# Optimization experiments

Measured on AMD Instinct MI355X. Metric: run time of the kernel, lower is better.

The kernel has to match this reference:

```python
import jax, jax.numpy as jnp
import numpy as np

B, N, F, H, L = 8, 4096, 240, 32, 240


def setup_inputs() -> dict:
    key = jax.random.key(0)
    k_x, k_a, k_w1, k_w2 = jax.random.split(key, 4)
    x = jax.random.normal(k_x, (B, N, F), dtype=jnp.float32)
    a = jax.random.uniform(k_a, (N, N), dtype=jnp.float32)
    W1 = jax.random.normal(k_w1, (F, H), dtype=jnp.float32) * (1.0 / np.sqrt(F))
    b1 = jnp.zeros((H,), dtype=jnp.float32)
    W2 = jax.random.normal(k_w2, (H, L), dtype=jnp.float32) * (1.0 / np.sqrt(H))
    b2 = jnp.zeros((L,), dtype=jnp.float32)
    return {"x": x, "a": a, "W1": W1, "b1": b1, "W2": W2, "b2": b2}


def reference(x, a, W1, b1, W2, b2):
    # GCNConv: transform features first (cheap), then aggregate over graph.
    h = jnp.einsum('bnf,fh->bnh', x, W1)            # [B, N, H]
    h = jnp.einsum('nm,bmh->bnh', a, h) + b1        # adjacency aggregation
    h = jax.nn.relu(h)
    # Dense linear head to label dim
    out = jnp.einsum('bnh,hl->bnl', h, W2) + b2     # [B, N, L]
    return out
```

## Files before the change

kernel.cpp:

```cpp
#include <hip/hip_runtime.h>
#include <hip/hip_bf16.h>

#define B_ 8
#define N_ 4096
#define F_ 240
#define H_ 32
#define L_ 240
#define C_ 256
#define KS 8
#define MT 64

typedef __attribute__((ext_vector_type(8))) short bf16x8;
typedef __attribute__((ext_vector_type(4))) short bf16x4;
typedef __attribute__((ext_vector_type(4))) float f32x4;

__device__ __forceinline__ short f2bf(float f) {
    union { float f; unsigned u; } v; v.f = f;
    unsigned r = (v.u + 0x7FFFu + ((v.u >> 16) & 1u)) >> 16;
    return (short)r;
}

__device__ __forceinline__ long hcf_sidx(int c, int m) {
    return ((long)(((((m >> 6) * 16 + (c >> 4)) * 2 + ((m >> 5) & 1)) * 64)
                   + ((m >> 3) & 3) * 16 + (c & 15))) * 8 + (m & 7);
}

__global__ __launch_bounds__(256) void stage1(const float* __restrict__ x,
                                              const float* __restrict__ W1,
                                              short* __restrict__ HcF) {
    __shared__ short w1t[32][264];
    __shared__ short xt[64][264];
    const int tid = threadIdx.x;
    const int b  = blockIdx.x >> 6;
    const int m0 = (blockIdx.x & 63) << 6;

    for (int idx = tid; idx < 240 * 32; idx += 256) {
        int f = idx >> 5, h = idx & 31;
        w1t[h][f] = f2bf(W1[idx]);
    }
    for (int idx = tid; idx < 32 * 16; idx += 256) {
        int h = idx >> 4, f = 240 + (idx & 15);
        w1t[h][f] = 0;
    }
    const float* xb = x + ((long)b * N_ + m0) * F_;
    for (int idx = tid; idx < 64 * 60; idx += 256) {
        int row = idx / 60, c4 = idx % 60;
        float4 v = *(const float4*)(xb + row * F_ + c4 * 4);
        bf16x4 s; s.x = f2bf(v.x); s.y = f2bf(v.y); s.z = f2bf(v.z); s.w = f2bf(v.w);
        *(bf16x4*)&xt[row][c4 * 4] = s;
    }
    for (int idx = tid; idx < 64 * 4; idx += 256) {
        int row = idx >> 2, f = 240 + (idx & 3) * 4;
        bf16x4 z = {0, 0, 0, 0};
        *(bf16x4*)&xt[row][f] = z;
    }
    __syncthreads();

    const int w = tid >> 6, lane = tid & 63, q = lane >> 4, r = lane & 15;
    f32x4 acc0 = {0,0,0,0}, acc1 = {0,0,0,0};
#pragma unroll
    for (int kk = 0; kk < 8; ++kk) {
        bf16x8 bfr = *(const bf16x8*)&xt[w * 16 + r][kk * 32 + q * 8];
        bf16x8 a0  = *(const bf16x8*)&w1t[r][kk * 32 + q * 8];
        bf16x8 a1  = *(const bf16x8*)&w1t[16 + r][kk * 32 + q * 8];
        acc0 = __builtin_amdgcn_mfma_f32_16x16x32_bf16(a0, bfr, acc0, 0, 0, 0);
        acc1 = __builtin_amdgcn_mfma_f32_16x16x32_bf16(a1, bfr, acc1, 0, 0, 0);
    }
    const int m = m0 + w * 16 + r;
#pragma unroll
    for (int reg = 0; reg < 4; ++reg) {
        int h0 = q * 4 + reg;
        HcF[hcf_sidx(b * 32 + h0, m)]      = f2bf(acc0[reg]);
        HcF[hcf_sidx(b * 32 + 16 + h0, m)] = f2bf(acc1[reg]);
    }
}

template <bool ATOMIC>
__global__ __launch_bounds__(256, 2) void stage2(const float* __restrict__ a,
                                                 const short* __restrict__ HcF,
                                                 float* __restrict__ P) {
    __shared__ short als[2][512 * 8];
    const int tid = threadIdx.x;
    const int bm = blockIdx.x >> 3;
    const int ks = blockIdx.x & 7;
    const int m0 = bm * MT;
    const int kb0 = ks * 8;

    const int w = tid >> 6, lane = tid & 63, q = lane >> 4, r = lane & 15;
    const bf16x8* __restrict__ Hv = (const bf16x8*)HcF;

    f32x4 acc[4][4];
#pragma unroll
    for (int i = 0; i < 4; ++i)
#pragma unroll
        for (int j = 0; j < 4; ++j) acc[i][j] = (f32x4){0, 0, 0, 0};

    float pre[16];
    const int f0i  = tid >> 7,        f1i  = (tid + 256) >> 7;
    const int f0kp = (tid >> 6) & 1,  f1kp = ((tid + 256) >> 6) & 1;
    const int f0q  = (tid >> 4) & 3,  f0r = tid & 15;

#define LOAD_A(kb)                                                             \
    {                                                                          \
        const float* s0 = a + (long)(m0 + f0i * 16 + f0r) * N_                 \
                            + (kb) * 64 + f0kp * 32 + f0q * 8;                 \
        const float* s1 = a + (long)(m0 + f1i * 16 + f0r) * N_                 \
                            + (kb) * 64 + f1kp * 32 + f0q * 8;                 \
        float4 v0 = *(const float4*)s0, v1 = *(const float4*)(s0 + 4);         \
        float4 v2 = *(const float4*)s1, v3 = *(const float4*)(s1 + 4);         \
        pre[0]=v0.x; pre[1]=v0.y; pre[2]=v0.z; pre[3]=v0.w;                    \
        pre[4]=v1.x; pre[5]=v1.y; pre[6]=v1.z; pre[7]=v1.w;                    \
        pre[8]=v2.x; pre[9]=v2.y; pre[10]=v2.z; pre[11]=v2.w;                  \
        pre[12]=v3.x; pre[13]=v3.y; pre[14]=v3.z; pre[15]=v3.w;                \
    }
#define STORE_A(buf)                                                           \
    {                                                                          \
        bf16x8 s0, s1;                                                         \
        _Pragma("unroll") for (int e = 0; e < 8; ++e) {                        \
            s0[e] = f2bf(pre[e]); s1[e] = f2bf(pre[8 + e]);                    \
        }                                                                      \
        *(bf16x8*)&als[buf][tid * 8]         = s0;                             \
        *(bf16x8*)&als[buf][(tid + 256) * 8] = s1;                             \
    }

    LOAD_A(kb0);
    STORE_A(0);

    bf16x8 bcur[8];
#pragma unroll
    for (int kp = 0; kp < 2; ++kp)
#pragma unroll
        for (int j = 0; j < 4; ++j)
            bcur[kp * 4 + j] = Hv[(long)((kb0 * 16 + w * 4 + j) * 2 + kp) * 64 + lane];

    __syncthreads();

    for (int t = 0; t < 8; ++t) {
        const int cur = t & 1;
        bf16x8 bnxt[8];
        if (t < 7) {
            LOAD_A(kb0 + t + 1);
#pragma unroll
            for (int kp = 0; kp < 2; ++kp)
#pragma unroll
                for (int j = 0; j < 4; ++j)
                    bnxt[kp * 4 + j] =
                        Hv[(long)(((kb0 + t + 1) * 16 + w * 4 + j) * 2 + kp) * 64 + lane];
        }
#pragma unroll
        for (int kp = 0; kp < 2; ++kp)
#pragma unroll
            for (int i = 0; i < 4; ++i) {
                bf16x8 af = *(const bf16x8*)&als[cur][((i * 2 + kp) * 64 + lane) * 8];
#pragma unroll
                for (int j = 0; j < 4; ++j)
                    acc[i][j] = __builtin_amdgcn_mfma_f32_16x16x32_bf16(
                        af, bcur[kp * 4 + j], acc[i][j], 0, 0, 0);
            }
        if (t < 7) {
            STORE_A(!cur);
#pragma unroll
            for (int u = 0; u < 8; ++u) bcur[u] = bnxt[u];
        }
        __syncthreads();
    }

#pragma unroll
    for (int i = 0; i < 4; ++i)
#pragma unroll
        for (int j = 0; j < 4; ++j) {
            const int c = w * 64 + j * 16 + r;
#pragma unroll
            for (int reg = 0; reg < 4; ++reg) {
                const int m = m0 + i * 16 + q * 4 + reg;
                if (ATOMIC) atomicAdd(&P[(long)m * C_ + c], acc[i][j][reg]);
                else        P[((long)ks * N_ + m) * C_ + c] = acc[i][j][reg];
            }
        }
#undef LOAD_A
#undef STORE_A
}

__global__ __launch_bounds__(256) void stage3(const float* __restrict__ P,
                                              const float* __restrict__ b1,
                                              const float* __restrict__ W2,
                                              const float* __restrict__ b2,
                                              float* __restrict__ out,
                                              int nks) {
    __shared__ float h2[32][36];
    const int tid = threadIdx.x;
    const int g0 = blockIdx.x * 32;
    const int b  = g0 >> 12;
    const int n0 = g0 & 4095;

    {
        const int rr = tid >> 3, c4 = tid & 7;
        const float* base = P + (long)(n0 + rr) * C_ + b * 32 + c4 * 4;
        f32x4 s = *(const f32x4*)base;
        for (int ks = 1; ks < nks; ++ks)
            s += *(const f32x4*)(base + (long)ks * (N_ * C_));
        s += *(const f32x4*)(b1 + c4 * 4);
        f32x4 z;
#pragma unroll
        for (int e = 0; e < 4; ++e) z[e] = s[e] > 0.f ? s[e] : 0.f;
        *(f32x4*)&h2[rr][c4 * 4] = z;
    }
    __syncthreads();

    if (tid < 240) {
        const int l = tid;
        float w2r[32];
#pragma unroll
        for (int h = 0; h < 32; ++h) w2r[h] = W2[h * 240 + l];
        const float bias = b2[l];
        for (int rr = 0; rr < 32; ++rr) {
            const f32x4* hv = (const f32x4*)h2[rr];
            float acc = bias;
#pragma unroll
            for (int hh = 0; hh < 8; ++hh) {
                f32x4 v = hv[hh];
                acc += v[0] * w2r[hh * 4 + 0];
                acc += v[1] * w2r[hh * 4 + 1];
                acc += v[2] * w2r[hh * 4 + 2];
                acc += v[3] * w2r[hh * 4 + 3];
            }
            out[(long)(g0 + rr) * 240 + l] = acc;
        }
    }
}

extern "C" void kernel_launch(void* const* d_in, const int* in_sizes, int n_in,
                              void* d_out, int out_size, void* d_ws, size_t ws_size,
                              hipStream_t stream) {
    const float* x  = (const float*)d_in[0];
    const float* a  = (const float*)d_in[1];
    const float* W1 = (const float*)d_in[2];
    const float* b1 = (const float*)d_in[3];
    const float* W2 = (const float*)d_in[4];
    const float* b2 = (const float*)d_in[5];
    float* out = (float*)d_out;

    short* HcF = (short*)d_ws;
    float* P   = (float*)((char*)d_ws + (size_t)C_ * N_ * 2);
    const size_t need = (size_t)C_ * N_ * 2 + (size_t)KS * N_ * C_ * 4;

    stage1<<<512, 256, 0, stream>>>(x, W1, HcF);
    if (ws_size >= need) {
        stage2<false><<<512, 256, 0, stream>>>(a, HcF, P);
        stage3<<<1024, 256, 0, stream>>>(P, b1, W2, b2, out, KS);
    } else {
        hipMemsetAsync(P, 0, (size_t)N_ * C_ * 4, stream);
        stage2<true><<<512, 256, 0, stream>>>(a, HcF, P);
        stage3<<<1024, 256, 0, stream>>>(P, b1, W2, b2, out, 1);
    }
}
```

Measured before the change: 171.4 us.

## Halve stage2 row tile to 32 and store split-K partials as bf16

Stage2 now processes 32 rows per block instead of 64, doubling the grid to 1024 blocks and raising the occupancy hint to 3, with a smaller LDS buffer and fewer accumulators per thread. The split-K partial sums are written as bf16 instead of fp32, halving the partial-buffer write and read traffic in stage2 and stage3. Stage3 is templated to accumulate either bf16 or fp32 partials. In exchange, each H tile is reloaded twice as often from global memory, the bf16 partials reduce precision, and no path runs if the workspace is too small even for the fp32 fallback.

```diff
diff --git a/kernel.cpp b/kernel.cpp
--- a/kernel.cpp
+++ b/kernel.cpp
@@ -8,7 +8,6 @@
 #define L_ 240
 #define C_ 256
 #define KS 8
-#define MT 64
 
 typedef __attribute__((ext_vector_type(8))) short bf16x8;
 typedef __attribute__((ext_vector_type(4))) short bf16x4;
@@ -18,6 +17,11 @@
     union { float f; unsigned u; } v; v.f = f;
     unsigned r = (v.u + 0x7FFFu + ((v.u >> 16) & 1u)) >> 16;
     return (short)r;
+}
+__device__ __forceinline__ float bf2f(short s) {
+    union { unsigned u; float f; } v;
+    v.u = ((unsigned)(unsigned short)s) << 16;
+    return v.f;
 }
 
 __device__ __forceinline__ long hcf_sidx(int c, int m) {
@@ -76,51 +80,41 @@
 }
 
 template <bool ATOMIC>
-__global__ __launch_bounds__(256, 2) void stage2(const float* __restrict__ a,
+__global__ __launch_bounds__(256, 3) void stage2(const float* __restrict__ a,
                                                  const short* __restrict__ HcF,
-                                                 float* __restrict__ P) {
-    __shared__ short als[2][512 * 8];
+                                                 void* __restrict__ Pv) {
+    __shared__ short als[2][256 * 8];
     const int tid = threadIdx.x;
     const int bm = blockIdx.x >> 3;
     const int ks = blockIdx.x & 7;
-    const int m0 = bm * MT;
+    const int m0 = bm * 32;
     const int kb0 = ks * 8;
 
     const int w = tid >> 6, lane = tid & 63, q = lane >> 4, r = lane & 15;
     const bf16x8* __restrict__ Hv = (const bf16x8*)HcF;
 
-    f32x4 acc[4][4];
-#pragma unroll
-    for (int i = 0; i < 4; ++i)
+    f32x4 acc[2][4];
+#pragma unroll
+    for (int i = 0; i < 2; ++i)
 #pragma unroll
         for (int j = 0; j < 4; ++j) acc[i][j] = (f32x4){0, 0, 0, 0};
 
-    float pre[16];
-    const int f0i  = tid >> 7,        f1i  = (tid + 256) >> 7;
-    const int f0kp = (tid >> 6) & 1,  f1kp = ((tid + 256) >> 6) & 1;
-    const int f0q  = (tid >> 4) & 3,  f0r = tid & 15;
+    float pre[8];
+    const int fi = tid >> 7, fkp = (tid >> 6) & 1, fq = (tid >> 4) & 3, fr = tid & 15;
 
 #define LOAD_A(kb)                                                             \
     {                                                                          \
-        const float* s0 = a + (long)(m0 + f0i * 16 + f0r) * N_                 \
-                            + (kb) * 64 + f0kp * 32 + f0q * 8;                 \
-        const float* s1 = a + (long)(m0 + f1i * 16 + f0r) * N_                 \
-                            + (kb) * 64 + f1kp * 32 + f0q * 8;                 \
-        float4 v0 = *(const float4*)s0, v1 = *(const float4*)(s0 + 4);         \
-        float4 v2 = *(const float4*)s1, v3 = *(const float4*)(s1 + 4);         \
+        const float* s = a + (long)(m0 + fi * 16 + fr) * N_                    \
+                           + (kb) * 64 + fkp * 32 + fq * 8;                    \
+        float4 v0 = *(const float4*)s, v1 = *(const float4*)(s + 4);           \
         pre[0]=v0.x; pre[1]=v0.y; pre[2]=v0.z; pre[3]=v0.w;                    \
         pre[4]=v1.x; pre[5]=v1.y; pre[6]=v1.z; pre[7]=v1.w;                    \
-        pre[8]=v2.x; pre[9]=v2.y; pre[10]=v2.z; pre[11]=v2.w;                  \
-        pre[12]=v3.x; pre[13]=v3.y; pre[14]=v3.z; pre[15]=v3.w;                \
     }
 #define STORE_A(buf)                                                           \
     {                                                                          \
-        bf16x8 s0, s1;                                                         \
-        _Pragma("unroll") for (int e = 0; e < 8; ++e) {                        \
-            s0[e] = f2bf(pre[e]); s1[e] = f2bf(pre[8 + e]);                    \
-        }                                                                      \
-        *(bf16x8*)&als[buf][tid * 8]         = s0;                             \
-        *(bf16x8*)&als[buf][(tid + 256) * 8] = s1;                             \
+        bf16x8 s0;                                                             \
+        _Pragma("unroll") for (int e = 0; e < 8; ++e) s0[e] = f2bf(pre[e]);    \
+        *(bf16x8*)&als[buf][tid * 8] = s0;                                     \
     }
 
     LOAD_A(kb0);
@@ -150,7 +144,7 @@
 #pragma unroll
         for (int kp = 0; kp < 2; ++kp)
 #pragma unroll
-            for (int i = 0; i < 4; ++i) {
+            for (int i = 0; i < 2; ++i) {
                 bf16x8 af = *(const bf16x8*)&als[cur][((i * 2 + kp) * 64 + lane) * 8];
 #pragma unroll
                 for (int j = 0; j < 4; ++j)
@@ -165,23 +159,39 @@
         __syncthreads();
     }
 
-#pragma unroll
-    for (int i = 0; i < 4; ++i)
-#pragma unroll
-        for (int j = 0; j < 4; ++j) {
-            const int c = w * 64 + j * 16 + r;
-#pragma unroll
-            for (int reg = 0; reg < 4; ++reg) {
-                const int m = m0 + i * 16 + q * 4 + reg;
-                if (ATOMIC) atomicAdd(&P[(long)m * C_ + c], acc[i][j][reg]);
-                else        P[((long)ks * N_ + m) * C_ + c] = acc[i][j][reg];
-            }
-        }
+    if (!ATOMIC) {
+        short* __restrict__ P = (short*)Pv;
+#pragma unroll
+        for (int i = 0; i < 2; ++i)
+#pragma unroll
+            for (int j = 0; j < 4; ++j) {
+                const int c = w * 64 + j * 16 + r;
+#pragma unroll
+                for (int reg = 0; reg < 4; ++reg) {
+                    const int m = m0 + i * 16 + q * 4 + reg;
+                    P[((long)ks * N_ + m) * C_ + c] = f2bf(acc[i][j][reg]);
+                }
+            }
+    } else {
+        float* __restrict__ P = (float*)Pv;
+#pragma unroll
+        for (int i = 0; i < 2; ++i)
+#pragma unroll
+            for (int j = 0; j < 4; ++j) {
+                const int c = w * 64 + j * 16 + r;
+#pragma unroll
+                for (int reg = 0; reg < 4; ++reg) {
+                    const int m = m0 + i * 16 + q * 4 + reg;
+                    atomicAdd(&P[(long)m * C_ + c], acc[i][j][reg]);
+                }
+            }
+    }
 #undef LOAD_A
 #undef STORE_A
 }
 
-__global__ __launch_bounds__(256) void stage3(const float* __restrict__ P,
+template <bool BF16P>
+__global__ __launch_bounds__(256) void stage3(const void* __restrict__ Pv,
                                               const float* __restrict__ b1,
                                               const float* __restrict__ W2,
                                               const float* __restrict__ b2,
@@ -194,16 +204,27 @@
     const int n0 = g0 & 4095;
 
     {
-        const int rr = tid >> 3, c4 = tid & 7;
-        const float* base = P + (long)(n0 + rr) * C_ + b * 32 + c4 * 4;
-        f32x4 s = *(const f32x4*)base;
-        for (int ks = 1; ks < nks; ++ks)
-            s += *(const f32x4*)(base + (long)ks * (N_ * C_));
-        s += *(const f32x4*)(b1 + c4 * 4);
-        f32x4 z;
-#pragma unroll
-        for (int e = 0; e < 4; ++e) z[e] = s[e] > 0.f ? s[e] : 0.f;
-        *(f32x4*)&h2[rr][c4 * 4] = z;
+        const int rr = tid >> 3, cg = tid & 7;
+        float s[4];
+        float4 bb = *(const float4*)(b1 + cg * 4);
+        s[0] = bb.x; s[1] = bb.y; s[2] = bb.z; s[3] = bb.w;
+        if (BF16P) {
+            const short* base = (const short*)Pv + (long)(n0 + rr) * C_ + b * 32 + cg * 4;
+            for (int ks = 0; ks < nks; ++ks) {
+                bf16x4 v = *(const bf16x4*)(base + (long)ks * (N_ * C_));
+#pragma unroll
+                for (int e = 0; e < 4; ++e) s[e] += bf2f(v[e]);
+            }
+        } else {
+            const float* base = (const float*)Pv + (long)(n0 + rr) * C_ + b * 32 + cg * 4;
+            for (int ks = 0; ks < nks; ++ks) {
+                f32x4 v = *(const f32x4*)(base + (long)ks * (N_ * C_));
+#pragma unroll
+                for (int e = 0; e < 4; ++e) s[e] += v[e];
+            }
+        }
+#pragma unroll
+        for (int e = 0; e < 4; ++e) h2[rr][cg * 4 + e] = s[e] > 0.f ? s[e] : 0.f;
     }
     __syncthreads();
 
@@ -241,16 +262,17 @@
     float* out = (float*)d_out;
 
     short* HcF = (short*)d_ws;
-    float* P   = (float*)((char*)d_ws + (size_t)C_ * N_ * 2);
-    const size_t need = (size_t)C_ * N_ * 2 + (size_t)KS * N_ * C_ * 4;
+    void*  P   = (void*)((char*)d_ws + (size_t)C_ * N_ * 2);
+    const size_t need_bf16 = (size_t)C_ * N_ * 2 + (size_t)KS * N_ * C_ * 2;
+    const size_t need_f32  = (size_t)C_ * N_ * 2 + (size_t)N_ * C_ * 4;
 
     stage1<<<512, 256, 0, stream>>>(x, W1, HcF);
-    if (ws_size >= need) {
-        stage2<false><<<512, 256, 0, stream>>>(a, HcF, P);
-        stage3<<<1024, 256, 0, stream>>>(P, b1, W2, b2, out, KS);
-    } else {
+    if (ws_size >= need_bf16) {
+        stage2<false><<<1024, 256, 0, stream>>>(a, HcF, P);
+        stage3<true><<<1024, 256, 0, stream>>>(P, b1, W2, b2, out, KS);
+    } else if (ws_size >= need_f32) {
         hipMemsetAsync(P, 0, (size_t)N_ * C_ * 4, stream);
-        stage2<true><<<512, 256, 0, stream>>>(a, HcF, P);
-        stage3<<<1024, 256, 0, stream>>>(P, b1, W2, b2, out, 1);
-    }
-}
+        stage2<true><<<1024, 256, 0, stream>>>(a, HcF, P);
+        stage3<false><<<1024, 256, 0, stream>>>(P, b1, W2, b2, out, 1);
+    }
+}
```

After: 170.8 us. No clear change (-0.3%).

## Store split-K partials as bf16 in fragment layout and use MFMA for output head

Applied to the files above, without the earlier changes.

Stage2 now writes its split-K partial sums as bf16 in a fragment-native layout instead of fp32, which halves the partial write and read traffic. It also deepens the register prefetch of the adjacency tile to two stages ahead and fully unrolls the k-loop. Stage3 reads the bf16 partials, applies bias and relu, and computes the W2 head with bf16 MFMA instead of scalar FMAs, and is reworked to 512-thread blocks. These steps add bf16 rounding to the partials and the hidden activations, and a separate fallback path keeps the atomic fp32 variant for small workspaces.

```diff
diff --git a/kernel.cpp b/kernel.cpp
--- a/kernel.cpp
+++ b/kernel.cpp
@@ -8,7 +8,6 @@
 #define L_ 240
 #define C_ 256
 #define KS 8
-#define MT 64
 
 typedef __attribute__((ext_vector_type(8))) short bf16x8;
 typedef __attribute__((ext_vector_type(4))) short bf16x4;
@@ -18,6 +17,11 @@
     union { float f; unsigned u; } v; v.f = f;
     unsigned r = (v.u + 0x7FFFu + ((v.u >> 16) & 1u)) >> 16;
     return (short)r;
+}
+__device__ __forceinline__ float bf2f(short s) {
+    union { unsigned u; float f; } v;
+    v.u = ((unsigned)(unsigned short)s) << 16;
+    return v.f;
 }
 
 __device__ __forceinline__ long hcf_sidx(int c, int m) {
@@ -75,16 +79,15 @@
     }
 }
 
-template <bool ATOMIC>
 __global__ __launch_bounds__(256, 2) void stage2(const float* __restrict__ a,
                                                  const short* __restrict__ HcF,
-                                                 float* __restrict__ P) {
+                                                 short* __restrict__ P) {
     __shared__ short als[2][512 * 8];
     const int tid = threadIdx.x;
     const int bm = blockIdx.x >> 3;
     const int ks = blockIdx.x & 7;
-    const int m0 = bm * MT;
-    const int kb0 = ks * 8;
+    const int m0 = bm << 6;
+    const int kb0 = ks << 3;
 
     const int w = tid >> 6, lane = tid & 63, q = lane >> 4, r = lane & 15;
     const bf16x8* __restrict__ Hv = (const bf16x8*)HcF;
@@ -95,51 +98,48 @@
 #pragma unroll
         for (int j = 0; j < 4; ++j) acc[i][j] = (f32x4){0, 0, 0, 0};
 
-    float pre[16];
-    const int f0i  = tid >> 7,        f1i  = (tid + 256) >> 7;
-    const int f0kp = (tid >> 6) & 1,  f1kp = ((tid + 256) >> 6) & 1;
-    const int f0q  = (tid >> 4) & 3,  f0r = tid & 15;
-
-#define LOAD_A(kb)                                                             \
+    const int fi = tid >> 7, fkp = (tid >> 6) & 1, fq = (tid >> 4) & 3, fr = tid & 15;
+    const float* aB0 = a + (long)(m0 + fi * 16 + fr) * N_ + (kb0 << 6) + fkp * 32 + fq * 8;
+    const float* aB1 = aB0 + 32 * N_;
+    float pre[2][16];
+
+#define LOAD_A(bk, t)                                                          \
     {                                                                          \
-        const float* s0 = a + (long)(m0 + f0i * 16 + f0r) * N_                 \
-                            + (kb) * 64 + f0kp * 32 + f0q * 8;                 \
-        const float* s1 = a + (long)(m0 + f1i * 16 + f0r) * N_                 \
-                            + (kb) * 64 + f1kp * 32 + f0q * 8;                 \
+        const float* s0 = aB0 + (t) * 64;                                      \
+        const float* s1 = aB1 + (t) * 64;                                      \
         float4 v0 = *(const float4*)s0, v1 = *(const float4*)(s0 + 4);         \
         float4 v2 = *(const float4*)s1, v3 = *(const float4*)(s1 + 4);         \
-        pre[0]=v0.x; pre[1]=v0.y; pre[2]=v0.z; pre[3]=v0.w;                    \
-        pre[4]=v1.x; pre[5]=v1.y; pre[6]=v1.z; pre[7]=v1.w;                    \
-        pre[8]=v2.x; pre[9]=v2.y; pre[10]=v2.z; pre[11]=v2.w;                  \
-        pre[12]=v3.x; pre[13]=v3.y; pre[14]=v3.z; pre[15]=v3.w;                \
-    }
-#define STORE_A(buf)                                                           \
+        pre[bk][0]=v0.x;  pre[bk][1]=v0.y;  pre[bk][2]=v0.z;  pre[bk][3]=v0.w; \
+        pre[bk][4]=v1.x;  pre[bk][5]=v1.y;  pre[bk][6]=v1.z;  pre[bk][7]=v1.w; \
+        pre[bk][8]=v2.x;  pre[bk][9]=v2.y;  pre[bk][10]=v2.z; pre[bk][11]=v2.w;\
+        pre[bk][12]=v3.x; pre[bk][13]=v3.y; pre[bk][14]=v3.z; pre[bk][15]=v3.w;\
+    }
+#define STORE_A(bk, buf)                                                       \
     {                                                                          \
         bf16x8 s0, s1;                                                         \
         _Pragma("unroll") for (int e = 0; e < 8; ++e) {                        \
-            s0[e] = f2bf(pre[e]); s1[e] = f2bf(pre[8 + e]);                    \
+            s0[e] = f2bf(pre[bk][e]); s1[e] = f2bf(pre[bk][8 + e]);            \
         }                                                                      \
         *(bf16x8*)&als[buf][tid * 8]         = s0;                             \
         *(bf16x8*)&als[buf][(tid + 256) * 8] = s1;                             \
     }
 
-    LOAD_A(kb0);
-    STORE_A(0);
-
-    bf16x8 bcur[8];
+    bf16x8 bcur[8], bnxt[8];
+    LOAD_A(0, 0);
+    LOAD_A(1, 1);
 #pragma unroll
     for (int kp = 0; kp < 2; ++kp)
 #pragma unroll
         for (int j = 0; j < 4; ++j)
             bcur[kp * 4 + j] = Hv[(long)((kb0 * 16 + w * 4 + j) * 2 + kp) * 64 + lane];
-
+    STORE_A(0, 0);
     __syncthreads();
 
+#pragma unroll
     for (int t = 0; t < 8; ++t) {
         const int cur = t & 1;
-        bf16x8 bnxt[8];
+        if (t < 6) LOAD_A(cur, t + 2);
         if (t < 7) {
-            LOAD_A(kb0 + t + 1);
 #pragma unroll
             for (int kp = 0; kp < 2; ++kp)
 #pragma unroll
@@ -151,62 +151,159 @@
         for (int kp = 0; kp < 2; ++kp)
 #pragma unroll
             for (int i = 0; i < 4; ++i) {
-                bf16x8 af = *(const bf16x8*)&als[cur][((i * 2 + kp) * 64 + lane) * 8];
+                bf16x8 af = *(const bf16x8*)&als[cur][(i * 128 + kp * 64 + lane) * 8];
 #pragma unroll
                 for (int j = 0; j < 4; ++j)
                     acc[i][j] = __builtin_amdgcn_mfma_f32_16x16x32_bf16(
                         af, bcur[kp * 4 + j], acc[i][j], 0, 0, 0);
             }
         if (t < 7) {
-            STORE_A(!cur);
+            STORE_A(!cur, !cur);
 #pragma unroll
             for (int u = 0; u < 8; ++u) bcur[u] = bnxt[u];
         }
         __syncthreads();
     }
 
+#pragma unroll
+    for (int i = 0; i < 4; ++i)
+#pragma unroll
+        for (int j = 0; j < 4; ++j) {
+            bf16x4 v;
+#pragma unroll
+            for (int reg = 0; reg < 4; ++reg) v[reg] = f2bf(acc[i][j][reg]);
+            const long F = (((long)ks * 64 + bm) * 4 + w) * 16 + i * 4 + j;
+            *(bf16x4*)&P[F * 256 + lane * 4] = v;
+        }
+#undef LOAD_A
+#undef STORE_A
+}
+
+__global__ __launch_bounds__(256, 2) void stage2_fb(const float* __restrict__ a,
+                                                    const short* __restrict__ HcF,
+                                                    float* __restrict__ P) {
+    __shared__ short als[512 * 8];
+    const int tid = threadIdx.x;
+    const int bm = blockIdx.x >> 3, ks = blockIdx.x & 7;
+    const int m0 = bm << 6, kb0 = ks << 3;
+    const int w = tid >> 6, lane = tid & 63, q = lane >> 4, r = lane & 15;
+    const bf16x8* __restrict__ Hv = (const bf16x8*)HcF;
+    f32x4 acc[4][4];
+#pragma unroll
+    for (int i = 0; i < 4; ++i)
+#pragma unroll
+        for (int j = 0; j < 4; ++j) acc[i][j] = (f32x4){0, 0, 0, 0};
+    const int fi = tid >> 7, fkp = (tid >> 6) & 1, fq = (tid >> 4) & 3, fr = tid & 15;
+    for (int t = 0; t < 8; ++t) {
+        __syncthreads();
+        for (int u = 0; u < 2; ++u) {
+            const float* s = a + (long)(m0 + (fi + 2 * u) * 16 + fr) * N_
+                               + ((kb0 + t) << 6) + fkp * 32 + fq * 8;
+            bf16x8 sv;
+            for (int e = 0; e < 8; ++e) sv[e] = f2bf(s[e]);
+            *(bf16x8*)&als[(tid + u * 256) * 8] = sv;
+        }
+        __syncthreads();
+#pragma unroll
+        for (int kp = 0; kp < 2; ++kp)
+#pragma unroll
+            for (int i = 0; i < 4; ++i) {
+                bf16x8 af = *(const bf16x8*)&als[(i * 128 + kp * 64 + lane) * 8];
+#pragma unroll
+                for (int j = 0; j < 4; ++j) {
+                    bf16x8 bfr = Hv[(long)(((kb0 + t) * 16 + w * 4 + j) * 2 + kp) * 64 + lane];
+                    acc[i][j] = __builtin_amdgcn_mfma_f32_16x16x32_bf16(af, bfr, acc[i][j], 0, 0, 0);
+                }
+            }
+    }
 #pragma unroll
     for (int i = 0; i < 4; ++i)
 #pragma unroll
         for (int j = 0; j < 4; ++j) {
             const int c = w * 64 + j * 16 + r;
 #pragma unroll
-            for (int reg = 0; reg < 4; ++reg) {
-                const int m = m0 + i * 16 + q * 4 + reg;
-                if (ATOMIC) atomicAdd(&P[(long)m * C_ + c], acc[i][j][reg]);
-                else        P[((long)ks * N_ + m) * C_ + c] = acc[i][j][reg];
-            }
-        }
-#undef LOAD_A
-#undef STORE_A
-}
-
-__global__ __launch_bounds__(256) void stage3(const float* __restrict__ P,
+            for (int reg = 0; reg < 4; ++reg)
+                atomicAdd(&P[(long)(m0 + i * 16 + q * 4 + reg) * C_ + c], acc[i][j][reg]);
+        }
+}
+
+__global__ __launch_bounds__(512) void stage3(const short* __restrict__ P,
                                               const float* __restrict__ b1,
                                               const float* __restrict__ W2,
                                               const float* __restrict__ b2,
-                                              float* __restrict__ out,
-                                              int nks) {
+                                              float* __restrict__ out) {
+    __shared__ short h2A[8][16][48];
+    __shared__ short W2T[240][56];
+    __shared__ float b2L[240];
+    const int tid = threadIdx.x;
+    const int bm = blockIdx.x >> 2, i = blockIdx.x & 3;
+    const int n0 = (bm << 6) + (i << 4);
+    const int w2 = tid >> 6, lane = tid & 63, q = lane >> 4, r = lane & 15;
+    const int w = w2 >> 1, jp = w2 & 1;
+
+    for (int idx = tid; idx < 240 * 32; idx += 512) {
+        int h = idx / 240, l = idx - h * 240;
+        W2T[l][h] = f2bf(W2[idx]);
+    }
+    if (tid < 240) b2L[tid] = b2[tid];
+
+#pragma unroll
+    for (int jj = 0; jj < 2; ++jj) {
+        const int j = jp * 2 + jj;
+        const int c = (w << 6) + (j << 4) + r;
+        const float bb = b1[c & 31];
+        float s[4] = {bb, bb, bb, bb};
+        const long F0 = ((long)bm * 4 + w) * 16 + i * 4 + j;
+#pragma unroll
+        for (int ks = 0; ks < 8; ++ks) {
+            bf16x4 v = *(const bf16x4*)&P[(F0 + (long)ks * 4096) * 256 + lane * 4];
+#pragma unroll
+            for (int e = 0; e < 4; ++e) s[e] += bf2f(v[e]);
+        }
+#pragma unroll
+        for (int e = 0; e < 4; ++e) {
+            float z = s[e] > 0.f ? s[e] : 0.f;
+            h2A[w2][q * 4 + e][(jj << 4) + r] = f2bf(z);
+        }
+    }
+    __syncthreads();
+
+    bf16x8 af = *(const bf16x8*)&h2A[w2][r][q * 8];
+    float* outB = out + ((long)w2 * N_ + n0) * 240;
+#pragma unroll
+    for (int lt = 0; lt < 15; ++lt) {
+        bf16x8 bf = *(const bf16x8*)&W2T[lt * 16 + r][q * 8];
+        f32x4 acc = {0, 0, 0, 0};
+        acc = __builtin_amdgcn_mfma_f32_16x16x32_bf16(af, bf, acc, 0, 0, 0);
+        const float bias = b2L[lt * 16 + r];
+#pragma unroll
+        for (int reg = 0; reg < 4; ++reg)
+            outB[(long)(q * 4 + reg) * 240 + lt * 16 + r] = acc[reg] + bias;
+    }
+}
+
+__global__ __launch_bounds__(256) void stage3_fb(const float* __restrict__ P,
+                                                 const float* __restrict__ b1,
+                                                 const float* __restrict__ W2,
+                                                 const float* __restrict__ b2,
+                                                 float* __restrict__ out) {
     __shared__ float h2[32][36];
     const int tid = threadIdx.x;
     const int g0 = blockIdx.x * 32;
     const int b  = g0 >> 12;
     const int n0 = g0 & 4095;
-
     {
-        const int rr = tid >> 3, c4 = tid & 7;
-        const float* base = P + (long)(n0 + rr) * C_ + b * 32 + c4 * 4;
-        f32x4 s = *(const f32x4*)base;
-        for (int ks = 1; ks < nks; ++ks)
-            s += *(const f32x4*)(base + (long)ks * (N_ * C_));
-        s += *(const f32x4*)(b1 + c4 * 4);
-        f32x4 z;
-#pragma unroll
-        for (int e = 0; e < 4; ++e) z[e] = s[e] > 0.f ? s[e] : 0.f;
-        *(f32x4*)&h2[rr][c4 * 4] = z;
+        const int rr = tid >> 3, cg = tid & 7;
+        const float* base = P + (long)(n0 + rr) * C_ + b * 32 + cg * 4;
+        f32x4 v = *(const f32x4*)base;
+        f32x4 bb = *(const f32x4*)(b1 + cg * 4);
+#pragma unroll
+        for (int e = 0; e < 4; ++e) {
+            float s = v[e] + bb[e];
+            h2[rr][cg * 4 + e] = s > 0.f ? s : 0.f;
+        }
     }
     __syncthreads();
-
     if (tid < 240) {
         const int l = tid;
         float w2r[32];
@@ -219,10 +316,8 @@
 #pragma unroll
             for (int hh = 0; hh < 8; ++hh) {
                 f32x4 v = hv[hh];
-                acc += v[0] * w2r[hh * 4 + 0];
-                acc += v[1] * w2r[hh * 4 + 1];
-                acc += v[2] * w2r[hh * 4 + 2];
-                acc += v[3] * w2r[hh * 4 + 3];
+                acc += v[0] * w2r[hh*4+0]; acc += v[1] * w2r[hh*4+1];
+                acc += v[2] * w2r[hh*4+2]; acc += v[3] * w2r[hh*4+3];
             }
             out[(long)(g0 + rr) * 240 + l] = acc;
         }
@@ -241,16 +336,17 @@
     float* out = (float*)d_out;
 
     short* HcF = (short*)d_ws;
-    float* P   = (float*)((char*)d_ws + (size_t)C_ * N_ * 2);
-    const size_t need = (size_t)C_ * N_ * 2 + (size_t)KS * N_ * C_ * 4;
+    void*  P   = (void*)((char*)d_ws + (size_t)C_ * N_ * 2);
+    const size_t need_main = (size_t)C_ * N_ * 2 + (size_t)KS * N_ * C_ * 2;
+    const size_t need_fb   = (size_t)C_ * N_ * 2 + (size_t)N_ * C_ * 4;
 
     stage1<<<512, 256, 0, stream>>>(x, W1, HcF);
-    if (ws_size >= need) {
-        stage2<false><<<512, 256, 0, stream>>>(a, HcF, P);
-        stage3<<<1024, 256, 0, stream>>>(P, b1, W2, b2, out, KS);
-    } else {
+    if (ws_size >= need_main) {
+        stage2<<<512, 256, 0, stream>>>(a, HcF, (short*)P);
+        stage3<<<256, 512, 0, stream>>>((const short*)P, b1, W2, b2, out);
+    } else if (ws_size >= need_fb) {
         hipMemsetAsync(P, 0, (size_t)N_ * C_ * 4, stream);
-        stage2<true><<<512, 256, 0, stream>>>(a, HcF, P);
-        stage3<<<1024, 256, 0, stream>>>(P, b1, W2, b2, out, 1);
-    }
-}
+        stage2_fb<<<512, 256, 0, stream>>>(a, HcF, (float*)P);
+        stage3_fb<<<1024, 256, 0, stream>>>((const float*)P, b1, W2, b2, out);
+    }
+}
```

After: 162.0 us. -5.5%, faster.
